# Kernel tuning notes

Hardware: AMD Instinct MI355X
Metric: run time of the kernel (lower is better)

Reference implementation:

```python
import jax, jax.numpy as jnp
import numpy as np

B, N, K, DIM = 1, 50000, 16, 64


def setup_inputs() -> dict:
    key = jax.random.key(0)
    ks = jax.random.split(key, 16)
    s = 0.05  # weight init scale
    return {
        "points_xyz": jax.random.normal(ks[0], (B, N, 3), jnp.float32),
        "points_features": jax.random.normal(ks[1], (B, N, DIM), jnp.float32),
        "neighbours_xyz": jax.random.normal(ks[2], (B, N, K, 3), jnp.float32),
        "neighbours_features": jax.random.normal(ks[3], (B, N, K, DIM), jnp.float32),
        "W_phi": jax.random.normal(ks[4], (DIM, DIM), jnp.float32) * s,
        "b_phi": jnp.zeros((DIM,), jnp.float32),
        "W_psi": jax.random.normal(ks[5], (DIM, DIM), jnp.float32) * s,
        "b_psi": jnp.zeros((DIM,), jnp.float32),
        "W_alpha": jax.random.normal(ks[6], (DIM, DIM), jnp.float32) * s,
        "b_alpha": jnp.zeros((DIM,), jnp.float32),
        "W_gamma": jax.random.normal(ks[7], (DIM, DIM), jnp.float32) * s,
        "b_gamma": jnp.zeros((DIM,), jnp.float32),
        "W_d1": jax.random.normal(ks[8], (3, DIM), jnp.float32) * s,
        "b_d1": jnp.zeros((DIM,), jnp.float32),
        "W_d2": jax.random.normal(ks[9], (DIM, DIM), jnp.float32) * s,
        "b_d2": jnp.zeros((DIM,), jnp.float32),
    }


def reference(points_xyz, points_features, neighbours_xyz, neighbours_features,
              W_phi, b_phi, W_psi, b_psi, W_alpha, b_alpha, W_gamma, b_gamma,
              W_d1, b_d1, W_d2, b_d2):
    # Positional encoding: delta(p_i - p_j) -> (B, N, K, DIM)
    diff = points_xyz[:, :, None, :] - neighbours_xyz          # (B,N,K,3)
    delta = jax.nn.relu((diff @ W_d1 + b_d1) @ W_d2 + b_d2)    # (B,N,K,DIM)

    phi = (points_features @ W_phi + b_phi)[:, :, None, :]     # (B,N,1,DIM)
    psi = neighbours_features @ W_psi + b_psi                  # (B,N,K,DIM)
    beta = phi - psi + delta                                   # (B,N,K,DIM)

    gamma_out = beta @ W_gamma + b_gamma                       # (B,N,K,DIM)
    # NOTE: faithful to source: softmax over the FEATURE axis (dim=-1)
    rho = jax.nn.softmax(gamma_out, axis=-1)                   # (B,N,K,DIM)

    alpha_out = neighbours_features @ W_alpha + b_alpha + delta  # (B,N,K,DIM)
    out = jnp.sum(rho * alpha_out, axis=2)                     # (B,N,DIM)
    return out
```

## Files before the change

kernel.cpp:

```cpp
#include <hip/hip_runtime.h>
#include <hip/hip_bf16.h>

typedef unsigned int uint_t;
typedef __attribute__((ext_vector_type(8))) short bf16x8;
typedef __attribute__((ext_vector_type(4))) float f32x4;

#define NPTS 50000
#define DIM  64
#define KNB  16
#define GPW  8
#define NGROUPS (NPTS / GPW)
#define WPB  4
#define NBLOCKS ((NGROUPS + WPB - 1) / WPB)

#define FR_WA    0
#define FR_PSIG  2048
#define FR_WG    4096
#define FR_PHIG  6144
#define WC4      8192
#define GB       8448
#define BA       8512

__device__ __forceinline__ uint_t pk(float a, float b) {
    union { __hip_bfloat162 h; uint_t u; } cv;
    cv.h = __float22bfloat162_rn(float2{a, b});
    return cv.u;
}

union Frag { uint_t u[4]; bf16x8 s; uint4 v; };

__device__ __forceinline__ int sigma(int k) {
    int t = k >> 1;
    return (t & 15) + 32 * (t >> 4) + 16 * (k & 1);
}

__global__ void pt_prep(const float* __restrict__ Wphi, const float* __restrict__ bphi,
                        const float* __restrict__ Wpsi, const float* __restrict__ bpsi,
                        const float* __restrict__ Wa,   const float* __restrict__ ba,
                        const float* __restrict__ Wg,   const float* __restrict__ bg,
                        const float* __restrict__ Wd1,  const float* __restrict__ bd1,
                        const float* __restrict__ Wd2,  const float* __restrict__ bd2,
                        float* __restrict__ ws) {
    int b = blockIdx.x, t = threadIdx.x;
    uint_t* wsu = (uint_t*)ws;
    if (b < 32) {
        int gid  = b * 256 + t;
        int img  = gid >> 11;
        int rem  = gid & 2047;
        int f    = rem >> 8;
        int lane = (rem >> 2) & 63;
        int w    = rem & 3;
        int k0   = (f & 1) * 32 + (lane >> 4) * 8 + 2 * w;
        int k1   = k0 + 1;
        int n    = (f >> 1) * 16 + (lane & 15);
        float v0, v1;
        if (img == 0) {
            v0 = Wa[k0 * 64 + n]; v1 = Wa[k1 * 64 + n];
            wsu[FR_WA + rem] = pk(v0, v1);
        } else if (img == 1) {
            float a0 = 0.f, a1 = 0.f;
            for (int c = 0; c < 64; ++c) {
                float wgc = Wg[c * 64 + n];
                a0 += Wpsi[k0 * 64 + c] * wgc;
                a1 += Wpsi[k1 * 64 + c] * wgc;
            }
            wsu[FR_PSIG + rem] = pk(-a0, -a1);
        } else if (img == 2) {
            v0 = Wg[sigma(k0) * 64 + n]; v1 = Wg[sigma(k1) * 64 + n];
            wsu[FR_WG + rem] = pk(v0, v1);
        } else {
            float a0 = 0.f, a1 = 0.f;
            for (int c = 0; c < 64; ++c) {
                float wgc = Wg[c * 64 + n];
                a0 += Wphi[k0 * 64 + c] * wgc;
                a1 += Wphi[k1 * 64 + c] * wgc;
            }
            wsu[FR_PHIG + rem] = pk(a0, a1);
        }
    } else if (t < 64) {
        float wx = 0.f, wy = 0.f, wz = 0.f;
        for (int m = 0; m < 64; ++m) {
            float w2 = Wd2[m * 64 + t];
            wx += Wd1[m] * w2;
            wy += Wd1[64 + m] * w2;
            wz += Wd1[128 + m] * w2;
        }
        float wb = bd2[t];
        for (int m = 0; m < 64; ++m) wb += bd1[m] * Wd2[m * 64 + t];
        ws[WC4 + t * 4 + 0] = wx;
        ws[WC4 + t * 4 + 1] = wy;
        ws[WC4 + t * 4 + 2] = wz;
        ws[WC4 + t * 4 + 3] = wb;
        float g = bg[t];
        for (int c = 0; c < 64; ++c) g += (bphi[c] - bpsi[c]) * Wg[c * 64 + t];
        ws[GB + t] = g;
        ws[BA + t] = ba[t];
    }
}

#define MFMA(A, B, C) __builtin_amdgcn_mfma_f32_16x16x32_bf16((A), (B), (C), 0, 0, 0)

#define WAREA 1224

__global__ __launch_bounds__(256, 2)
void pt_main(const float* __restrict__ pxyz, const float* __restrict__ pfeat,
             const float* __restrict__ nxyz, const float* __restrict__ nfeat,
             const float* __restrict__ ws,   float* __restrict__ out) {
    __shared__ float lds[WPB][WAREA];

    const int t    = threadIdx.x;
    const int wv   = t >> 6;
    const int lane = t & 63;
    const int c16  = lane & 15;
    const int quad = lane >> 4;

    const int g = blockIdx.x * WPB + wv;
    if (g >= NGROUPS) return;

    float*  phig_s = &lds[wv][0];
    uint_t* utr    = (uint_t*)(phig_s + 520);
    float*  dxyz   = (float*)(utr + 544);
    float*  pxyz_s = dxyz + 128;

    const uint4* fr = (const uint4*)ws;
    Frag wa[8], wpsig[8], wg[8];
    #pragma unroll
    for (int f = 0; f < 8; ++f) {
        wa[f].v    = fr[           f * 64 + lane];
        wpsig[f].v = fr[ 512 +     f * 64 + lane];
        wg[f].v    = fr[1024 +     f * 64 + lane];
    }
    float4 wc[4];
    float ba_r[4], gbr[4];
    #pragma unroll
    for (int nt = 0; nt < 4; ++nt) {
        int d = nt * 16 + c16;
        wc[nt]   = ((const float4*)(ws + WC4))[d];
        ba_r[nt] = ws[BA + d];
        gbr[nt]  = ws[GB + d];
    }

    const int g0 = g * GPW;
    const int k3 = lane / 3, c3 = lane - k3 * 3;

    if (lane < 24) pxyz_s[lane] = pxyz[g0 * 3 + lane];
    float nv0 = (lane < 48) ? nxyz[(size_t)g0 * 48 + lane] : 0.f;
    if (lane < 48) dxyz[k3 * 4 + c3] = pxyz_s[c3] - nv0;

    {
        float4 x0{}, x1{}, x2{}, x3{};
        if (c16 < 8) {
            const float* base = pfeat + (size_t)(g0 + c16) * 64 + quad * 8;
            x0 = *(const float4*)(base);
            x1 = *(const float4*)(base + 4);
            x2 = *(const float4*)(base + 32);
            x3 = *(const float4*)(base + 36);
        }
        Frag pa0, pa1;
        pa0.u[0] = pk(x0.x, x0.y); pa0.u[1] = pk(x0.z, x0.w);
        pa0.u[2] = pk(x1.x, x1.y); pa0.u[3] = pk(x1.z, x1.w);
        pa1.u[0] = pk(x2.x, x2.y); pa1.u[1] = pk(x2.z, x2.w);
        pa1.u[2] = pk(x3.x, x3.y); pa1.u[3] = pk(x3.z, x3.w);
        #pragma unroll
        for (int nt = 0; nt < 4; ++nt) {
            Frag b0, b1;
            b0.v = fr[1536 + (nt * 2 + 0) * 64 + lane];
            b1.v = fr[1536 + (nt * 2 + 1) * 64 + lane];
            f32x4 acc = {gbr[nt], gbr[nt], gbr[nt], gbr[nt]};
            acc = MFMA(pa0.s, b0.s, acc);
            acc = MFMA(pa1.s, b1.s, acc);
            if (quad < 2) {
                #pragma unroll
                for (int r = 0; r < 4; ++r)
                    phig_s[(quad * 4 + r) * 65 + nt * 16 + c16] = acc[r];
            }
        }
    }

    const float* nfb = nfeat + (size_t)g0 * (KNB * 64) + (size_t)c16 * 64 + quad * 8;
    float4 f0 = *(const float4*)(nfb);
    float4 f1 = *(const float4*)(nfb + 4);
    float4 f2 = *(const float4*)(nfb + 32);
    float4 f3 = *(const float4*)(nfb + 36);
    float nvn = (lane < 48) ? nxyz[(size_t)g0 * 48 + 48 + lane] : 0.f;

    #pragma unroll 1
    for (int i = 0; i < GPW; ++i) {
        const int n = g0 + i;

        Frag na0, na1;
        na0.u[0] = pk(f0.x, f0.y); na0.u[1] = pk(f0.z, f0.w);
        na0.u[2] = pk(f1.x, f1.y); na0.u[3] = pk(f1.z, f1.w);
        na1.u[0] = pk(f2.x, f2.y); na1.u[1] = pk(f2.z, f2.w);
        na1.u[2] = pk(f3.x, f3.y); na1.u[3] = pk(f3.z, f3.w);
        if (i + 1 < GPW) {
            const float* nf2 = nfb + (size_t)(i + 1) * (KNB * 64);
            f0 = *(const float4*)(nf2);
            f1 = *(const float4*)(nf2 + 4);
            f2 = *(const float4*)(nf2 + 32);
            f3 = *(const float4*)(nf2 + 36);
        }

        float ph[4];
        #pragma unroll
        for (int nt = 0; nt < 4; ++nt) ph[nt] = phig_s[i * 65 + nt * 16 + c16];
        float4 dd[4];
        #pragma unroll
        for (int r = 0; r < 4; ++r)
            dd[r] = ((const float4*)dxyz)[(i & 1) * 16 + quad * 4 + r];

        if (i + 1 < GPW) {
            if (lane < 48)
                dxyz[((i + 1) & 1) * 64 + k3 * 4 + c3] = pxyz_s[(i + 1) * 3 + c3] - nvn;
            if (i + 2 < GPW)
                nvn = (lane < 48) ? nxyz[((size_t)n + 2) * 48 + lane] : 0.f;
        }

        float d_c[4][4];
        #pragma unroll
        for (int nt = 0; nt < 4; ++nt) {
            #pragma unroll
            for (int r = 0; r < 4; ++r) {
                float u = fmaf(dd[r].x, wc[nt].x,
                          fmaf(dd[r].y, wc[nt].y,
                          fmaf(dd[r].z, wc[nt].z, wc[nt].w)));
                d_c[nt][r] = fmaxf(u, 0.f);
            }
        }
        #pragma unroll
        for (int r = 0; r < 4; ++r) {
            int row = (quad * 4 + r) * 34;
            utr[row + c16]      = pk(d_c[0][r], d_c[1][r]);
            utr[row + 16 + c16] = pk(d_c[2][r], d_c[3][r]);
        }

        f32x4 aacc[4];
        #pragma unroll
        for (int nt = 0; nt < 4; ++nt) {
            aacc[nt] = f32x4{ba_r[nt], ba_r[nt], ba_r[nt], ba_r[nt]};
            aacc[nt] = MFMA(na0.s, wa[nt * 2 + 0].s, aacc[nt]);
            aacc[nt] = MFMA(na1.s, wa[nt * 2 + 1].s, aacc[nt]);
        }
        f32x4 gacc[4];
        #pragma unroll
        for (int nt = 0; nt < 4; ++nt) {
            gacc[nt] = f32x4{ph[nt], ph[nt], ph[nt], ph[nt]};
            gacc[nt] = MFMA(na0.s, wpsig[nt * 2 + 0].s, gacc[nt]);
            gacc[nt] = MFMA(na1.s, wpsig[nt * 2 + 1].s, gacc[nt]);
        }
        Frag da0, da1;
        {
            const uint_t* rowp = utr + c16 * 34 + quad * 4;
            uint2 a = *(const uint2*)(rowp);
            uint2 b = *(const uint2*)(rowp + 2);
            uint2 c = *(const uint2*)(rowp + 16);
            uint2 d = *(const uint2*)(rowp + 18);
            da0.u[0] = a.x; da0.u[1] = a.y; da0.u[2] = b.x; da0.u[3] = b.y;
            da1.u[0] = c.x; da1.u[1] = c.y; da1.u[2] = d.x; da1.u[3] = d.y;
        }
        #pragma unroll
        for (int nt = 0; nt < 4; ++nt) {
            gacc[nt] = MFMA(da0.s, wg[nt * 2 + 0].s, gacc[nt]);
            gacc[nt] = MFMA(da1.s, wg[nt * 2 + 1].s, gacc[nt]);
        }
        #pragma unroll
        for (int nt = 0; nt < 4; ++nt)
            #pragma unroll
            for (int r = 0; r < 4; ++r) aacc[nt][r] += d_c[nt][r];

        float e[4][4], smi[4];
        #pragma unroll
        for (int r = 0; r < 4; ++r) {
            float s = 0.f;
            #pragma unroll
            for (int nt = 0; nt < 4; ++nt) { e[nt][r] = __expf(gacc[nt][r]); s += e[nt][r]; }
            #pragma unroll
            for (int d2 = 1; d2 < 16; d2 <<= 1) s += __shfl_xor(s, d2);
            smi[r] = __builtin_amdgcn_rcpf(s);
        }
        float p0 = 0.f, p1 = 0.f, p2 = 0.f, p3 = 0.f;
        #pragma unroll
        for (int r = 0; r < 4; ++r) {
            p0 = fmaf(e[0][r] * smi[r], aacc[0][r], p0);
            p1 = fmaf(e[1][r] * smi[r], aacc[1][r], p1);
            p2 = fmaf(e[2][r] * smi[r], aacc[2][r], p2);
            p3 = fmaf(e[3][r] * smi[r], aacc[3][r], p3);
        }
        p0 += __shfl_xor(p0, 16); p0 += __shfl_xor(p0, 32);
        p1 += __shfl_xor(p1, 16); p1 += __shfl_xor(p1, 32);
        p2 += __shfl_xor(p2, 16); p2 += __shfl_xor(p2, 32);
        p3 += __shfl_xor(p3, 16); p3 += __shfl_xor(p3, 32);
        float sel = (quad == 0) ? p0 : (quad == 1) ? p1 : (quad == 2) ? p2 : p3;
        out[(size_t)n * 64 + lane] = sel;
    }
}

extern "C" void kernel_launch(void* const* d_in, const int* in_sizes, int n_in,
                              void* d_out, int out_size, void* d_ws, size_t ws_size,
                              hipStream_t stream) {
    const float* pxyz  = (const float*)d_in[0];
    const float* pfeat = (const float*)d_in[1];
    const float* nxyz  = (const float*)d_in[2];
    const float* nfeat = (const float*)d_in[3];
    const float* Wphi  = (const float*)d_in[4];
    const float* bphi  = (const float*)d_in[5];
    const float* Wpsi  = (const float*)d_in[6];
    const float* bpsi  = (const float*)d_in[7];
    const float* Wa    = (const float*)d_in[8];
    const float* ba    = (const float*)d_in[9];
    const float* Wg    = (const float*)d_in[10];
    const float* bg    = (const float*)d_in[11];
    const float* Wd1   = (const float*)d_in[12];
    const float* bd1   = (const float*)d_in[13];
    const float* Wd2   = (const float*)d_in[14];
    const float* bd2   = (const float*)d_in[15];
    float* ws = (float*)d_ws;

    pt_prep<<<33, 256, 0, stream>>>(Wphi, bphi, Wpsi, bpsi, Wa, ba, Wg, bg,
                                    Wd1, bd1, Wd2, bd2, ws);
    pt_main<<<NBLOCKS, 256, 0, stream>>>(pxyz, pfeat, nxyz, nfeat, ws, (float*)d_out);
}
```

Before: 346.9 us.

## Stage MFMA weight fragments in LDS and raise occupancy target

Weight fragments for the alpha, psi and gamma MFMAs (24 uint4 per lane) are now loaded once per block into shared memory and re-read from LDS right before each MFMA, instead of being held in registers for the whole kernel. This frees many VGPRs, which lets launch_bounds ask for 3 blocks per CU instead of 2 and hide more global-load latency. In exchange it adds LDS reads in the inner loop, uses 24KB more LDS per block, and adds a block-wide barrier before the early-exit check.

```diff
diff --git a/kernel.cpp b/kernel.cpp
--- a/kernel.cpp
+++ b/kernel.cpp
@@ -102,10 +102,11 @@
 
 #define WAREA 1224
 
-__global__ __launch_bounds__(256, 2)
+__global__ __launch_bounds__(256, 3)
 void pt_main(const float* __restrict__ pxyz, const float* __restrict__ pfeat,
              const float* __restrict__ nxyz, const float* __restrict__ nfeat,
              const float* __restrict__ ws,   float* __restrict__ out) {
+    __shared__ uint4 wfr[1536];
     __shared__ float lds[WPB][WAREA];
 
     const int t    = threadIdx.x;
@@ -115,6 +116,13 @@
     const int quad = lane >> 4;
 
     const int g = blockIdx.x * WPB + wv;
+
+    const uint4* fr = (const uint4*)ws;
+    #pragma unroll
+    for (int idx = 0; idx < 6; ++idx)
+        wfr[idx * 256 + t] = fr[idx * 256 + t];
+    __syncthreads();
+
     if (g >= NGROUPS) return;
 
     float*  phig_s = &lds[wv][0];
@@ -122,14 +130,8 @@
     float*  dxyz   = (float*)(utr + 544);
     float*  pxyz_s = dxyz + 128;
 
-    const uint4* fr = (const uint4*)ws;
-    Frag wa[8], wpsig[8], wg[8];
-    #pragma unroll
-    for (int f = 0; f < 8; ++f) {
-        wa[f].v    = fr[           f * 64 + lane];
-        wpsig[f].v = fr[ 512 +     f * 64 + lane];
-        wg[f].v    = fr[1024 +     f * 64 + lane];
-    }
+    const uint4* wfl = wfr + lane;
+
     float4 wc[4];
     float ba_r[4], gbr[4];
     #pragma unroll
@@ -237,16 +239,22 @@
         f32x4 aacc[4];
         #pragma unroll
         for (int nt = 0; nt < 4; ++nt) {
+            Frag w0, w1;
+            w0.v = wfl[(nt * 2 + 0) * 64];
+            w1.v = wfl[(nt * 2 + 1) * 64];
             aacc[nt] = f32x4{ba_r[nt], ba_r[nt], ba_r[nt], ba_r[nt]};
-            aacc[nt] = MFMA(na0.s, wa[nt * 2 + 0].s, aacc[nt]);
-            aacc[nt] = MFMA(na1.s, wa[nt * 2 + 1].s, aacc[nt]);
+            aacc[nt] = MFMA(na0.s, w0.s, aacc[nt]);
+            aacc[nt] = MFMA(na1.s, w1.s, aacc[nt]);
         }
         f32x4 gacc[4];
         #pragma unroll
         for (int nt = 0; nt < 4; ++nt) {
+            Frag w0, w1;
+            w0.v = wfl[512 + (nt * 2 + 0) * 64];
+            w1.v = wfl[512 + (nt * 2 + 1) * 64];
             gacc[nt] = f32x4{ph[nt], ph[nt], ph[nt], ph[nt]};
-            gacc[nt] = MFMA(na0.s, wpsig[nt * 2 + 0].s, gacc[nt]);
-            gacc[nt] = MFMA(na1.s, wpsig[nt * 2 + 1].s, gacc[nt]);
+            gacc[nt] = MFMA(na0.s, w0.s, gacc[nt]);
+            gacc[nt] = MFMA(na1.s, w1.s, gacc[nt]);
         }
         Frag da0, da1;
         {
@@ -260,8 +268,11 @@
         }
         #pragma unroll
         for (int nt = 0; nt < 4; ++nt) {
-            gacc[nt] = MFMA(da0.s, wg[nt * 2 + 0].s, gacc[nt]);
-            gacc[nt] = MFMA(da1.s, wg[nt * 2 + 1].s, gacc[nt]);
+            Frag w0, w1;
+            w0.v = wfl[1024 + (nt * 2 + 0) * 64];
+            w1.v = wfl[1024 + (nt * 2 + 1) * 64];
+            gacc[nt] = MFMA(da0.s, w0.s, gacc[nt]);
+            gacc[nt] = MFMA(da1.s, w1.s, gacc[nt]);
         }
         #pragma unroll
         for (int nt = 0; nt < 4; ++nt)
```

Measured after the change: 467.4 us. 1.35x slower.

## Stage neighbour features into LDS via async global_load_lds triple buffer

Applied to the files above, without the earlier changes.

Neighbour features and xyz for each point are now copied straight into a three-slot per-wave LDS ring with global_load_lds, two points ahead, guarded by explicit vmcnt waits. A swizzled layout avoids bank conflicts when the MFMA operands are read back. Per-point output stores are collected in an LDS buffer and written once at the end with coalesced float4 stores. This deepens prefetch and frees registers, at the cost of a much larger LDS footprint per wave, which may lower occupancy, and fragile hand-counted waitcnt values.

```diff
diff --git a/kernel.cpp b/kernel.cpp
--- a/kernel.cpp
+++ b/kernel.cpp
@@ -100,7 +100,39 @@
 
 #define MFMA(A, B, C) __builtin_amdgcn_mfma_f32_16x16x32_bf16((A), (B), (C), 0, 0, 0)
 
-#define WAREA 1224
+#define O_PHIG 0
+#define O_UTR  520
+#define O_DXY  1064
+#define O_PXY  1128
+#define O_OBUF 1160
+#define O_NF   1672
+#define NFSLOT 1088
+#define WAREA  (O_NF + 3 * NFSLOT)
+
+__device__ __forceinline__ void gl_lds16(const void* g, void* l) {
+    __builtin_amdgcn_global_load_lds(
+        (const __attribute__((address_space(1))) unsigned int*)g,
+        (__attribute__((address_space(3))) unsigned int*)l, 16, 0, 0);
+}
+__device__ __forceinline__ void gl_lds4(const void* g, void* l) {
+    __builtin_amdgcn_global_load_lds(
+        (const __attribute__((address_space(1))) unsigned int*)g,
+        (__attribute__((address_space(3))) unsigned int*)l, 4, 0, 0);
+}
+
+__device__ __forceinline__ void stage_pt(const float* __restrict__ nfeat,
+                                         const float* __restrict__ nxyz,
+                                         int p, float* ldsbase,
+                                         const int* soff, int lane) {
+    const char* sp = (const char*)nfeat + (size_t)p * 4096;
+    gl_lds16(sp + soff[0], ldsbase);
+    gl_lds16(sp + soff[1], ldsbase + 256);
+    gl_lds16(sp + soff[2], ldsbase + 512);
+    gl_lds16(sp + soff[3], ldsbase + 768);
+    int xi = p * 48 + lane;
+    if (xi > NPTS * KNB * 3 - 1) xi = NPTS * KNB * 3 - 1;
+    gl_lds4(nxyz + xi, ldsbase + 1024);
+}
 
 __global__ __launch_bounds__(256, 2)
 void pt_main(const float* __restrict__ pxyz, const float* __restrict__ pfeat,
@@ -117,18 +149,34 @@
     const int g = blockIdx.x * WPB + wv;
     if (g >= NGROUPS) return;
 
-    float*  phig_s = &lds[wv][0];
-    uint_t* utr    = (uint_t*)(phig_s + 520);
-    float*  dxyz   = (float*)(utr + 544);
-    float*  pxyz_s = dxyz + 128;
+    float*  W      = lds[wv];
+    float*  phig_s = W + O_PHIG;
+    uint_t* utr    = (uint_t*)(W + O_UTR);
+    float*  dxyz   = W + O_DXY;
+    float*  pxyz_s = W + O_PXY;
+    float*  obuf   = W + O_OBUF;
+    float*  nfl    = W + O_NF;
+
+    const int g0 = g * GPW;
+    const int k3 = lane / 3, c3 = lane - k3 * 3;
+
+    int soff[4];
+    #pragma unroll
+    for (int j = 0; j < 4; ++j) {
+        int row = j * 4 + quad;
+        soff[j] = row * 256 + (((c16 - row) & 15) << 4);
+    }
+
+    stage_pt(nfeat, nxyz, g0,     nfl + 0 * NFSLOT, soff, lane);
+    stage_pt(nfeat, nxyz, g0 + 1, nfl + 1 * NFSLOT, soff, lane);
 
     const uint4* fr = (const uint4*)ws;
     Frag wa[8], wpsig[8], wg[8];
     #pragma unroll
     for (int f = 0; f < 8; ++f) {
-        wa[f].v    = fr[           f * 64 + lane];
-        wpsig[f].v = fr[ 512 +     f * 64 + lane];
-        wg[f].v    = fr[1024 +     f * 64 + lane];
+        wa[f].v    = fr[        f * 64 + lane];
+        wpsig[f].v = fr[ 512 +  f * 64 + lane];
+        wg[f].v    = fr[1024 +  f * 64 + lane];
     }
     float4 wc[4];
     float ba_r[4], gbr[4];
@@ -140,12 +188,7 @@
         gbr[nt]  = ws[GB + d];
     }
 
-    const int g0 = g * GPW;
-    const int k3 = lane / 3, c3 = lane - k3 * 3;
-
     if (lane < 24) pxyz_s[lane] = pxyz[g0 * 3 + lane];
-    float nv0 = (lane < 48) ? nxyz[(size_t)g0 * 48 + lane] : 0.f;
-    if (lane < 48) dxyz[k3 * 4 + c3] = pxyz_s[c3] - nv0;
 
     {
         float4 x0{}, x1{}, x2{}, x3{};
@@ -177,29 +220,41 @@
         }
     }
 
-    const float* nfb = nfeat + (size_t)g0 * (KNB * 64) + (size_t)c16 * 64 + quad * 8;
-    float4 f0 = *(const float4*)(nfb);
-    float4 f1 = *(const float4*)(nfb + 4);
-    float4 f2 = *(const float4*)(nfb + 32);
-    float4 f3 = *(const float4*)(nfb + 36);
-    float nvn = (lane < 48) ? nxyz[(size_t)g0 * 48 + 48 + lane] : 0.f;
-
+    int slot = 0;
     #pragma unroll 1
     for (int i = 0; i < GPW; ++i) {
         const int n = g0 + i;
 
+        if (i + 2 < GPW) {
+            int s2 = slot + 2; if (s2 >= 3) s2 -= 3;
+            stage_pt(nfeat, nxyz, n + 2, nfl + s2 * NFSLOT, soff, lane);
+        }
+        __builtin_amdgcn_sched_barrier(0);
+        if (i < GPW - 2)       { asm volatile("s_waitcnt vmcnt(10)" ::: "memory"); }
+        else if (i == GPW - 2) { asm volatile("s_waitcnt vmcnt(5)"  ::: "memory"); }
+        else                   { asm volatile("s_waitcnt vmcnt(0)"  ::: "memory"); }
+        __builtin_amdgcn_sched_barrier(0);
+
+        const float* nfp = nfl + slot * NFSLOT;
+
+        if (lane < 48) {
+            float v = nfp[1024 + lane];
+            dxyz[k3 * 4 + c3] = pxyz_s[i * 3 + c3] - v;
+        }
+
+        int b0 = c16 * 64 + (((quad * 2     + c16) & 15) << 2);
+        int b1 = c16 * 64 + (((quad * 2 + 1 + c16) & 15) << 2);
+        int b2 = c16 * 64 + (((quad * 2 + 8 + c16) & 15) << 2);
+        int b3 = c16 * 64 + (((quad * 2 + 9 + c16) & 15) << 2);
+        float4 x0 = *(const float4*)(nfp + b0);
+        float4 x1 = *(const float4*)(nfp + b1);
+        float4 x2 = *(const float4*)(nfp + b2);
+        float4 x3 = *(const float4*)(nfp + b3);
         Frag na0, na1;
-        na0.u[0] = pk(f0.x, f0.y); na0.u[1] = pk(f0.z, f0.w);
-        na0.u[2] = pk(f1.x, f1.y); na0.u[3] = pk(f1.z, f1.w);
-        na1.u[0] = pk(f2.x, f2.y); na1.u[1] = pk(f2.z, f2.w);
-        na1.u[2] = pk(f3.x, f3.y); na1.u[3] = pk(f3.z, f3.w);
-        if (i + 1 < GPW) {
-            const float* nf2 = nfb + (size_t)(i + 1) * (KNB * 64);
-            f0 = *(const float4*)(nf2);
-            f1 = *(const float4*)(nf2 + 4);
-            f2 = *(const float4*)(nf2 + 32);
-            f3 = *(const float4*)(nf2 + 36);
-        }
+        na0.u[0] = pk(x0.x, x0.y); na0.u[1] = pk(x0.z, x0.w);
+        na0.u[2] = pk(x1.x, x1.y); na0.u[3] = pk(x1.z, x1.w);
+        na1.u[0] = pk(x2.x, x2.y); na1.u[1] = pk(x2.z, x2.w);
+        na1.u[2] = pk(x3.x, x3.y); na1.u[3] = pk(x3.z, x3.w);
 
         float ph[4];
         #pragma unroll
@@ -207,14 +262,7 @@
         float4 dd[4];
         #pragma unroll
         for (int r = 0; r < 4; ++r)
-            dd[r] = ((const float4*)dxyz)[(i & 1) * 16 + quad * 4 + r];
-
-        if (i + 1 < GPW) {
-            if (lane < 48)
-                dxyz[((i + 1) & 1) * 64 + k3 * 4 + c3] = pxyz_s[(i + 1) * 3 + c3] - nvn;
-            if (i + 2 < GPW)
-                nvn = (lane < 48) ? nxyz[((size_t)n + 2) * 48 + lane] : 0.f;
-        }
+            dd[r] = ((const float4*)dxyz)[quad * 4 + r];
 
         float d_c[4][4];
         #pragma unroll
@@ -291,8 +339,16 @@
         p2 += __shfl_xor(p2, 16); p2 += __shfl_xor(p2, 32);
         p3 += __shfl_xor(p3, 16); p3 += __shfl_xor(p3, 32);
         float sel = (quad == 0) ? p0 : (quad == 1) ? p1 : (quad == 2) ? p2 : p3;
-        out[(size_t)n * 64 + lane] = sel;
-    }
+        obuf[i * 64 + lane] = sel;
+
+        slot = (slot == 2) ? 0 : slot + 1;
+    }
+
+    float4 o0 = ((const float4*)obuf)[lane * 2];
+    float4 o1 = ((const float4*)obuf)[lane * 2 + 1];
+    float4* og = (float4*)(out + (size_t)g0 * 64);
+    og[lane * 2]     = o0;
+    og[lane * 2 + 1] = o1;
 }
 
 extern "C" void kernel_launch(void* const* d_in, const int* in_sizes, int n_in,
```

Measured after the change: 351.3 us. No clear change (+1.3%).

## Coalesce neighbour feature loads via bpermute shuffle and stage output in LDS

Applied to the files above, without the earlier changes.

Neighbour feature loads now read 16-byte chunks at a stride that makes consecutive lanes more contiguous in memory. ds_bpermute then rearranges the packed bf16 words into the K-split layout the MFMA expects. Per-point output rows are buffered in LDS and written once per group as wide float4 stores. This cuts global memory transactions at the cost of 16 extra bpermutes per point and more LDS per wave, which may reduce occupancy.

```diff
diff --git a/kernel.cpp b/kernel.cpp
--- a/kernel.cpp
+++ b/kernel.cpp
@@ -100,7 +100,11 @@
 
 #define MFMA(A, B, C) __builtin_amdgcn_mfma_f32_16x16x32_bf16((A), (B), (C), 0, 0, 0)
 
-#define WAREA 1224
+#define WAREA 1736
+
+__device__ __forceinline__ uint_t bperm(int byteaddr, uint_t v) {
+    return (uint_t)__builtin_amdgcn_ds_bpermute(byteaddr, (int)v);
+}
 
 __global__ __launch_bounds__(256, 2)
 void pt_main(const float* __restrict__ pxyz, const float* __restrict__ pfeat,
@@ -121,6 +125,7 @@
     uint_t* utr    = (uint_t*)(phig_s + 520);
     float*  dxyz   = (float*)(utr + 544);
     float*  pxyz_s = dxyz + 128;
+    float*  obuf   = pxyz_s + 32;
 
     const uint4* fr = (const uint4*)ws;
     Frag wa[8], wpsig[8], wg[8];
@@ -177,28 +182,43 @@
         }
     }
 
-    const float* nfb = nfeat + (size_t)g0 * (KNB * 64) + (size_t)c16 * 64 + quad * 8;
+    const float* nfb = nfeat + (size_t)g0 * (KNB * 64) + (size_t)c16 * 64 + quad * 4;
     float4 f0 = *(const float4*)(nfb);
-    float4 f1 = *(const float4*)(nfb + 4);
+    float4 f1 = *(const float4*)(nfb + 16);
     float4 f2 = *(const float4*)(nfb + 32);
-    float4 f3 = *(const float4*)(nfb + 36);
+    float4 f3 = *(const float4*)(nfb + 48);
     float nvn = (lane < 48) ? nxyz[(size_t)g0 * 48 + 48 + lane] : 0.f;
+
+    const int s0 = ((((quad & 1) << 1) << 4) + c16) << 2;
+    const int s1 = s0 + 64;
 
     #pragma unroll 1
     for (int i = 0; i < GPW; ++i) {
         const int n = g0 + i;
 
-        Frag na0, na1;
-        na0.u[0] = pk(f0.x, f0.y); na0.u[1] = pk(f0.z, f0.w);
-        na0.u[2] = pk(f1.x, f1.y); na0.u[3] = pk(f1.z, f1.w);
-        na1.u[0] = pk(f2.x, f2.y); na1.u[1] = pk(f2.z, f2.w);
-        na1.u[2] = pk(f3.x, f3.y); na1.u[3] = pk(f3.z, f3.w);
+        uint_t p0w0 = pk(f0.x, f0.y), p0w1 = pk(f0.z, f0.w);
+        uint_t p1w0 = pk(f1.x, f1.y), p1w1 = pk(f1.z, f1.w);
+        uint_t p2w0 = pk(f2.x, f2.y), p2w1 = pk(f2.z, f2.w);
+        uint_t p3w0 = pk(f3.x, f3.y), p3w1 = pk(f3.z, f3.w);
         if (i + 1 < GPW) {
             const float* nf2 = nfb + (size_t)(i + 1) * (KNB * 64);
             f0 = *(const float4*)(nf2);
-            f1 = *(const float4*)(nf2 + 4);
+            f1 = *(const float4*)(nf2 + 16);
             f2 = *(const float4*)(nf2 + 32);
-            f3 = *(const float4*)(nf2 + 36);
+            f3 = *(const float4*)(nf2 + 48);
+        }
+
+        Frag na0, na1;
+        {
+            uint_t a, b;
+            a = bperm(s0, p0w0); b = bperm(s0, p1w0); na0.u[0] = (quad < 2) ? a : b;
+            a = bperm(s0, p0w1); b = bperm(s0, p1w1); na0.u[1] = (quad < 2) ? a : b;
+            a = bperm(s1, p0w0); b = bperm(s1, p1w0); na0.u[2] = (quad < 2) ? a : b;
+            a = bperm(s1, p0w1); b = bperm(s1, p1w1); na0.u[3] = (quad < 2) ? a : b;
+            a = bperm(s0, p2w0); b = bperm(s0, p3w0); na1.u[0] = (quad < 2) ? a : b;
+            a = bperm(s0, p2w1); b = bperm(s0, p3w1); na1.u[1] = (quad < 2) ? a : b;
+            a = bperm(s1, p2w0); b = bperm(s1, p3w0); na1.u[2] = (quad < 2) ? a : b;
+            a = bperm(s1, p2w1); b = bperm(s1, p3w1); na1.u[3] = (quad < 2) ? a : b;
         }
 
         float ph[4];
@@ -291,8 +311,14 @@
         p2 += __shfl_xor(p2, 16); p2 += __shfl_xor(p2, 32);
         p3 += __shfl_xor(p3, 16); p3 += __shfl_xor(p3, 32);
         float sel = (quad == 0) ? p0 : (quad == 1) ? p1 : (quad == 2) ? p2 : p3;
-        out[(size_t)n * 64 + lane] = sel;
-    }
+        obuf[i * 64 + lane] = sel;
+    }
+
+    float4 o0 = ((const float4*)obuf)[lane * 2];
+    float4 o1 = ((const float4*)obuf)[lane * 2 + 1];
+    float4* og = (float4*)(out + (size_t)g0 * 64);
+    og[lane * 2]     = o0;
+    og[lane * 2 + 1] = o1;
 }
 
 extern "C" void kernel_launch(void* const* d_in, const int* in_sizes, int n_in,
```

Result: slower. 354.0 us (+2.0%).
